# Kernel tuning notes

Measured on AMD Instinct MI355X. Metric: run time of the kernel, lower is better.

The kernel has to match this reference:

```python
import jax, jax.numpy as jnp
import numpy as np

HEADS = 16


def bemm(x, weight, bias, er, es):
    # BatchEnsembleMM.forward: x [T,B,Hin], weight [Hout,Hin], er [B,Hin], es [B,Hout]
    x_r = x * er[None, :, :]
    x_mm = jnp.einsum('tbh,oh->tbo', x_r, weight)
    return x_mm * es[None, :, :] + bias


def rel_shift(x):
    # RelativeShift.forward (batch_first): x [N, len_q, len_r]
    n, q, r = x.shape
    x_pad = jnp.pad(x, ((0, 0), (0, 0), (1, 0)))        # [N, q, r+1]
    x_view = x_pad.reshape(n, r + 1, q)[:, 1:, :]        # drop first 'row'
    return x_view.reshape(n, q, r)


def setup_inputs() -> dict:
    key = jax.random.key(0)
    ks = jax.random.split(key, 14)
    T, B, H = 1024, 8, 1024
    Lr = 1024
    s = 0.02
    return {
        'inputs': jax.random.normal(ks[0], (T, B, H), jnp.float32),
        'pos': jax.random.normal(ks[1], (Lr, 1, H), jnp.float32),
        'input_weights': jax.random.normal(ks[2], (3 * H, H), jnp.float32) * s,
        'input_biases': jax.random.normal(ks[3], (3 * H,), jnp.float32) * s,
        'pos_weights': jax.random.normal(ks[4], (H, H), jnp.float32) * s,
        'pos_biases': jax.random.normal(ks[5], (H,), jnp.float32) * s,
        'output_weights': jax.random.normal(ks[6], (H, H), jnp.float32) * s,
        'output_biases': jax.random.normal(ks[7], (H,), jnp.float32) * s,
        'r_i': 1.0 + jax.random.normal(ks[8], (B, H), jnp.float32) * 0.1,
        's_i': 1.0 + jax.random.normal(ks[9], (B, 3 * H), jnp.float32) * 0.1,
        'r_p': 1.0 + jax.random.normal(ks[10], (B, H), jnp.float32) * 0.1,
        's_p': 1.0 + jax.random.normal(ks[11], (B, H), jnp.float32) * 0.1,
        'r_w_bias': jax.random.normal(ks[12], (HEADS, H // HEADS), jnp.float32) * s,
        'r_r_bias': jax.random.normal(ks[13], (HEADS, H // HEADS), jnp.float32) * s,
        'heads': HEADS,
    }


def reference(inputs, pos, input_weights, input_biases, pos_weights, pos_biases,
              output_weights, output_biases, r_i, s_i, r_p, s_p,
              r_w_bias, r_r_bias, heads):
    T, B, H = inputs.shape
    hd = H // heads
    scale = hd ** (-0.5)
    Lr = pos.shape[0]

    pos_rep = jnp.broadcast_to(pos, (Lr, B, H))

    # BatchEnsemble QKV and positional projections (training path)
    qkv = bemm(inputs, input_weights, input_biases, r_i, s_i)       # [T,B,3H]
    qkv = qkv.reshape(T, B * heads, 3, hd)
    queries, keys, values = qkv[:, :, 0, :], qkv[:, :, 1, :], qkv[:, :, 2, :]

    r_head_k = bemm(pos_rep, pos_weights, pos_biases, r_p, s_p)     # [Lr,B,H]
    r_head_k = r_head_k.reshape(Lr, B * heads, hd)

    rw_head_q = (queries.reshape(T, B, heads, hd) + r_w_bias).reshape(T, B * heads, hd)
    rr_head_q = (queries.reshape(T, B, heads, hd) + r_r_bias).reshape(T, B * heads, hd)

    # content score AC and position score BD
    matmul_ac = jnp.einsum('qnd,knd->nqk', rw_head_q, keys) * scale    # [B*h,T,T]
    matmul_bd = jnp.einsum('qnd,rnd->nqr', rr_head_q, r_head_k) * scale
    matmul_bd = rel_shift(matmul_bd)[:, :, :T]

    attn_score = matmul_ac + matmul_bd
    softmax_results = jax.nn.softmax(attn_score.astype(jnp.float32), axis=-1).astype(inputs.dtype)

    context = jnp.einsum('nqk,knd->qnd', softmax_results, values).reshape(T, B, H)
    outputs = jnp.einsum('tbh,oh->tbo', context, output_weights) + output_biases
    return outputs
```

## Files before the change

### kernel.cpp

```cpp
#include <hip/hip_runtime.h>
#include <cstdint>
#include <cstddef>

using u16 = unsigned short;
typedef short short8 __attribute__((ext_vector_type(8)));
typedef unsigned short us8 __attribute__((ext_vector_type(8)));
typedef unsigned short us4 __attribute__((ext_vector_type(4)));
typedef float f32x4 __attribute__((ext_vector_type(4)));
typedef float f4 __attribute__((ext_vector_type(4)));

#define T_ 1024
#define B_ 8
#define H_ 1024
#define HEADS_ 16
#define HD_ 64
#define N3_ 3072

__device__ __forceinline__ float b2f(u16 u){
  union { float f; unsigned int i; } v; v.i = ((unsigned int)u) << 16; return v.f;
}
__device__ __forceinline__ u16 f2b(float f){
  union { float f; unsigned int i; } v; v.f = f;
  return (u16)((v.i + 0x8000u) >> 16);
}

template<bool HAS_S, bool SCALE_A, bool POS_A, bool A_BF16, bool OUT_F32>
__global__ __launch_bounds__(256) void k_gemm(const void* __restrict__ A_, const float* __restrict__ W,
                                              const float* __restrict__ RA, const float* __restrict__ S,
                                              const float* __restrict__ bias, void* __restrict__ C_, int N){
  const int K = 1024;
  const int n0 = blockIdx.x * 128, m0 = blockIdx.y * 128;
  const int tid = threadIdx.x, lane = tid & 63;
  const int wave = tid >> 6, wr = wave >> 1, wc = wave & 1;
  __shared__ alignas(16) u16 At[128 * 32];
  __shared__ alignas(16) u16 Bt[128 * 32];
  f32x4 acc[4][4] = {};

  for (int kt = 0; kt < 32; ++kt){
    const int k0 = kt * 32;
    f4 wv[4];
    us8 avb[2];
    f4 avf[4];
#pragma unroll
    for (int i = 0; i < 4; ++i){
      int c = tid + i * 256, r = c >> 3, sg = c & 7;
      wv[i] = *(const f4*)(W + (size_t)(n0 + r) * K + k0 + sg * 4);
    }
    if (A_BF16){
      const u16* A = (const u16*)A_;
#pragma unroll
      for (int i = 0; i < 2; ++i){
        int c = tid + i * 256, r = c >> 2, sg = c & 3;
        avb[i] = *(const us8*)(A + (size_t)(m0 + r) * K + k0 + sg * 8);
      }
    } else {
      const float* A = (const float*)A_;
#pragma unroll
      for (int i = 0; i < 4; ++i){
        int c = tid + i * 256, r = c >> 3, sg = c & 7;
        int m = m0 + r;
        const float* ap = POS_A ? (A + (size_t)(m >> 3) * K + k0 + sg * 4)
                                : (A + (size_t)m * K + k0 + sg * 4);
        avf[i] = *(const f4*)ap;
        if (SCALE_A){
          f4 rv = *(const f4*)(RA + (m & 7) * K + k0 + sg * 4);
          avf[i] = avf[i] * rv;
        }
      }
    }
    __syncthreads();
#pragma unroll
    for (int i = 0; i < 4; ++i){
      int c = tid + i * 256, r = c >> 3, sg = c & 7;
      us4 pw;
#pragma unroll
      for (int u = 0; u < 4; ++u) pw[u] = f2b(wv[i][u]);
      *(us4*)(Bt + r * 32 + sg * 4) = pw;
    }
    if (A_BF16){
#pragma unroll
      for (int i = 0; i < 2; ++i){
        int c = tid + i * 256, r = c >> 2, sg = c & 3;
        *(us8*)(At + r * 32 + sg * 8) = avb[i];
      }
    } else {
#pragma unroll
      for (int i = 0; i < 4; ++i){
        int c = tid + i * 256, r = c >> 3, sg = c & 7;
        us4 pa;
#pragma unroll
        for (int u = 0; u < 4; ++u) pa[u] = f2b(avf[i][u]);
        *(us4*)(At + r * 32 + sg * 4) = pa;
      }
    }
    __syncthreads();
    short8 af[4], bf[4];
#pragma unroll
    for (int i = 0; i < 4; ++i){
      int ar = wr * 64 + i * 16 + (lane & 15);
      af[i] = *(const short8*)(At + ar * 32 + ((lane >> 4) << 3));
      int br = wc * 64 + i * 16 + (lane & 15);
      bf[i] = *(const short8*)(Bt + br * 32 + ((lane >> 4) << 3));
    }
#pragma unroll
    for (int i = 0; i < 4; ++i)
#pragma unroll
      for (int j = 0; j < 4; ++j)
        acc[i][j] = __builtin_amdgcn_mfma_f32_16x16x32_bf16(af[i], bf[j], acc[i][j], 0, 0, 0);
  }
#pragma unroll
  for (int i = 0; i < 4; ++i){
    int row0 = wr * 64 + i * 16 + ((lane >> 4) << 2);
#pragma unroll
    for (int j = 0; j < 4; ++j){
      int o = n0 + wc * 64 + j * 16 + (lane & 15);
      float bv = bias[o];
#pragma unroll
      for (int jj = 0; jj < 4; ++jj){
        int m = m0 + row0 + jj;
        float v = acc[i][j][jj];
        if (HAS_S) v *= S[(m & 7) * N + o];
        v += bv;
        if (OUT_F32) ((float*)C_)[(size_t)m * N + o] = v;
        else         ((u16*)C_)[(size_t)m * N + o] = f2b(v);
      }
    }
  }
}

__global__ __launch_bounds__(256) void k_vt(const u16* __restrict__ qkv, u16* __restrict__ VT){
  const int tt = blockIdx.x;
  const int n = blockIdx.y;
  const int b = n >> 4, head = n & 15;
  __shared__ alignas(16) u16 tile[64][72];
  const int tid = threadIdx.x;
#pragma unroll
  for (int i = 0; i < 2; ++i){
    int c = tid + i * 256;
    int r = c >> 3, sg = c & 7;
    const u16* src = qkv + ((size_t)(tt * 64 + r) * 8 + b) * N3_ + head * 192 + 128 + sg * 8;
    *(us8*)&tile[r][sg * 8] = *(const us8*)src;
  }
  __syncthreads();
#pragma unroll
  for (int i = 0; i < 2; ++i){
    int c = tid + i * 256;
    int d = c >> 3, sg = c & 7;
    us8 ov;
#pragma unroll
    for (int u = 0; u < 8; ++u) ov[u] = tile[sg * 8 + u][d];
    *(us8*)(VT + ((size_t)n * 64 + d) * 1024 + tt * 64 + sg * 8) = ov;
  }
}

#define G_OFF   0
#define KV_OFF  67856
#define RWQ_OFF 133392
#define RRQ_OFF 137488
#define RED_OFF 143632
#define SMEM_SZ 145808

__device__ __forceinline__ int gswz(int byt){ return byt ^ (((byt >> 13) & 3) << 5); }

__global__ __launch_bounds__(512, 1) void k_attn(const u16* __restrict__ qkv, const u16* __restrict__ rk,
                                                 const u16* __restrict__ VTg, const float* __restrict__ rwb,
                                                 const float* __restrict__ rrb, u16* __restrict__ ctx){
  const int bid = blockIdx.x;
  const int n = (bid & 7) + ((bid >> 8) << 3);
  const int qb = (bid >> 3) & 31;
  const int q0 = qb * 32;
  const int bat = n >> 4, head = n & 15;
  const int tid = threadIdx.x, lane = tid & 63, wave = tid >> 6;
  const int l15 = lane & 15, grp = lane >> 4;

  __shared__ alignas(16) char smem[SMEM_SZ];
  char* gB  = smem + G_OFF;
  char* kvS = smem + KV_OFF;
  u16* rwq = (u16*)(smem + RWQ_OFF);
  u16* rrq = (u16*)(smem + RRQ_OFF);
  float* redf = (float*)(smem + RED_OFF);

  us8 stv[8];

#pragma unroll
  for (int i = 0; i < 8; ++i){ int c = tid + i * 512, r = c >> 3, sg = c & 7;
    stv[i] = *(const us8*)(rk + ((size_t)r * 8 + bat) * 1024 + head * 64 + sg * 8); }

  const float PRESCALE = 0.125f * 1.44269504089f;
#pragma unroll
  for (int rep = 0; rep < 2; ++rep){
    int c = tid + rep * 512;
    if (c < 640){
      int s = c >> 3, sg = c & 7;
      u16* dst; int row; const float* bias;
      if (s < 32){ dst = rwq; row = s; bias = rwb; }
      else       { dst = rrq; row = s - 32; bias = rrb; }
      int qrow = q0 + row;
      float v[8];
      const float* bp2 = bias + head * 64 + sg * 8;
      if (qrow < T_){
        const u16* qp = qkv + ((size_t)qrow * 8 + bat) * N3_ + head * 192 + sg * 8;
        us8 qv = *(const us8*)qp;
        f4 b0 = *(const f4*)bp2, b1 = *(const f4*)(bp2 + 4);
#pragma unroll
        for (int u = 0; u < 4; ++u){
          v[u]     = (b2f(qv[u])     + b0[u]) * PRESCALE;
          v[u + 4] = (b2f(qv[u + 4]) + b1[u]) * PRESCALE;
        }
      } else {
#pragma unroll
        for (int u = 0; u < 8; ++u) v[u] = 0.f;
      }
      us8 pk;
#pragma unroll
      for (int u = 0; u < 8; ++u) pk[u] = f2b(v[u]);
      *(us8*)((char*)dst + row * 128 + ((sg * 16) ^ ((row & 7) << 4))) = pk;
    }
  }
  if (tid < 33) *(u16*)(gB + gswz(tid * 2050 + 2048)) = 0;

  auto ldf = [&](const void* base, int row, int kkb)->short8 {
    int co = kkb + (grp << 4);
    return *(const short8*)((const char*)base + row * 128 + (co ^ ((row & 7) << 4)));
  };
  auto stageKV = [&](){
#pragma unroll
    for (int i = 0; i < 8; ++i){ int c = tid + i * 512, r = c >> 3, sg = c & 7;
      *(us8*)(kvS + r * 128 + ((sg * 16) ^ ((r & 7) << 4))) = stv[i]; }
  };
  auto computeB = [&](int s){
    short8 af[3][2];
#pragma unroll
    for (int pi = 0; pi < 3; ++pi)
#pragma unroll
      for (int kk = 0; kk < 2; ++kk) af[pi][kk] = ldf(rrq, pi * 16 + l15, kk * 64);
#pragma unroll
    for (int c4 = 0; c4 < 4; ++c4){
      int brow = wave * 64 + c4 * 16 + l15;
      short8 bf0 = ldf(kvS, brow, 0), bf1 = ldf(kvS, brow, 64);
      int rg = s * 512 + wave * 64 + c4 * 16 + l15;
#pragma unroll
      for (int pi = 0; pi < 3; ++pi){
        f32x4 acc = {0.f, 0.f, 0.f, 0.f};
        acc = __builtin_amdgcn_mfma_f32_16x16x32_bf16(af[pi][0], bf0, acc, 0, 0, 0);
        acc = __builtin_amdgcn_mfma_f32_16x16x32_bf16(af[pi][1], bf1, acc, 0, 0, 0);
#pragma unroll
        for (int jj = 0; jj < 4; ++jj){
          int a = pi * 16 + (grp << 2) + jj;
          if (a < 33) *(u16*)(gB + gswz(a * 2050 + (rg << 1))) = f2b(acc[jj]);
        }
      }
    }
  };

  __syncthreads();
  stageKV();
#pragma unroll
  for (int i = 0; i < 8; ++i){ int c = tid + i * 512, r = c >> 3, sg = c & 7;
    stv[i] = *(const us8*)(rk + ((size_t)(512 + r) * 8 + bat) * 1024 + head * 64 + sg * 8); }
  __syncthreads();
  computeB(0);
  __syncthreads();
  stageKV();
#pragma unroll
  for (int i = 0; i < 8; ++i){ int c = tid + i * 512, r = c >> 3, sg = c & 7;
    stv[i] = *(const us8*)(qkv + ((size_t)r * 8 + bat) * N3_ + head * 192 + 64 + sg * 8); }
  __syncthreads();
  computeB(1);

  f32x4 p[2][2][4];
  float pm[2][4];
#pragma unroll
  for (int m = 0; m < 2; ++m)
#pragma unroll
    for (int jj = 0; jj < 4; ++jj) pm[m][jj] = -3.0e38f;

  auto computeC = [&](int s){
    short8 af[2][2];
#pragma unroll
    for (int m = 0; m < 2; ++m)
#pragma unroll
      for (int kk = 0; kk < 2; ++kk) af[m][kk] = ldf(rwq, m * 16 + l15, kk * 64);
#pragma unroll
    for (int c4 = 0; c4 < 4; ++c4){
      int brow = wave * 64 + c4 * 16 + l15;
      short8 bf0 = ldf(kvS, brow, 0), bf1 = ldf(kvS, brow, 64);
      int bcol = s * 512 + wave * 64 + c4 * 16 + l15;
      int byt0 = ((1023 - q0 + bcol) << 1) + (grp << 13);
#pragma unroll
      for (int m = 0; m < 2; ++m){
        f32x4 acc = {0.f, 0.f, 0.f, 0.f};
        acc = __builtin_amdgcn_mfma_f32_16x16x32_bf16(af[m][0], bf0, acc, 0, 0, 0);
        acc = __builtin_amdgcn_mfma_f32_16x16x32_bf16(af[m][1], bf1, acc, 0, 0, 0);
#pragma unroll
        for (int jj = 0; jj < 4; ++jj){
          int byt = byt0 + (m << 15) + (jj << 11);
          float gv = b2f(*(const u16*)(gB + gswz(byt)));
          float sc = acc[jj] + gv;
          p[s][m][c4][jj] = sc;
          pm[m][jj] = fmaxf(pm[m][jj], sc);
        }
      }
    }
  };

  __syncthreads();
  stageKV();
#pragma unroll
  for (int i = 0; i < 8; ++i){ int c = tid + i * 512, r = c >> 3, sg = c & 7;
    stv[i] = *(const us8*)(qkv + ((size_t)(512 + r) * 8 + bat) * N3_ + head * 192 + 64 + sg * 8); }
  __syncthreads();
  computeC(0);
  __syncthreads();
  stageKV();
  __syncthreads();
  computeC(1);

#pragma unroll
  for (int m = 0; m < 2; ++m)
#pragma unroll
    for (int jj = 0; jj < 4; ++jj)
#pragma unroll
      for (int mk = 1; mk < 16; mk <<= 1) pm[m][jj] = fmaxf(pm[m][jj], __shfl_xor(pm[m][jj], mk));
  __syncthreads();
#pragma unroll
  for (int i = 0; i < 8; ++i){ int c = tid + i * 512, d = c >> 6, tc = c & 63;
    stv[i] = *(const us8*)(VTg + ((size_t)n * 64 + d) * 1024 + tc * 8); }
  if (l15 == 0){
#pragma unroll
    for (int m = 0; m < 2; ++m)
#pragma unroll
      for (int jj = 0; jj < 4; ++jj) redf[wave * 32 + m * 16 + (grp << 2) + jj] = pm[m][jj];
  }
  __syncthreads();
  float M_[2][4];
#pragma unroll
  for (int m = 0; m < 2; ++m)
#pragma unroll
    for (int jj = 0; jj < 4; ++jj){
      int row = m * 16 + (grp << 2) + jj;
      float v = redf[row];
#pragma unroll
      for (int w = 1; w < 8; ++w) v = fmaxf(v, redf[w * 32 + row]);
      M_[m][jj] = v;
    }
#pragma unroll
  for (int i = 0; i < 8; ++i){ int c = tid + i * 512, d = c >> 6, tc = c & 63;
    *(us8*)(kvS + d * 1024 + ((tc * 16) ^ ((d & 31) << 4))) = stv[i]; }
#pragma unroll
  for (int i = 0; i < 8; ++i){ int c = tid + i * 512, d = c >> 6, tc = c & 63;
    stv[i] = *(const us8*)(VTg + ((size_t)n * 64 + d) * 1024 + 512 + tc * 8); }

  float L_[2][4] = {};
#pragma unroll
  for (int s = 0; s < 2; ++s)
#pragma unroll
    for (int m = 0; m < 2; ++m)
#pragma unroll
      for (int c4 = 0; c4 < 4; ++c4)
#pragma unroll
        for (int jj = 0; jj < 4; ++jj){
          float e = __builtin_exp2f(p[s][m][c4][jj] - M_[m][jj]);
          p[s][m][c4][jj] = e;
          L_[m][jj] += e;
        }
#pragma unroll
  for (int m = 0; m < 2; ++m)
#pragma unroll
    for (int jj = 0; jj < 4; ++jj)
#pragma unroll
      for (int mk = 1; mk < 16; mk <<= 1) L_[m][jj] += __shfl_xor(L_[m][jj], mk);
  if (l15 == 0){
#pragma unroll
    for (int m = 0; m < 2; ++m)
#pragma unroll
      for (int jj = 0; jj < 4; ++jj) redf[256 + wave * 32 + m * 16 + (grp << 2) + jj] = L_[m][jj];
  }
  __syncthreads();
  if (wave == 0 && l15 == 0){
#pragma unroll
    for (int m = 0; m < 2; ++m)
#pragma unroll
      for (int jj = 0; jj < 4; ++jj){
        int row = m * 16 + (grp << 2) + jj;
        float sum = 0.f;
#pragma unroll
        for (int w = 0; w < 8; ++w) sum += redf[256 + w * 32 + row];
        redf[512 + row] = 1.0f / (sum + 1e-20f);
      }
  }

  char* ptW = smem + G_OFF + wave * 8192;
#pragma unroll
  for (int s = 0; s < 2; ++s)
#pragma unroll
    for (int m = 0; m < 2; ++m)
#pragma unroll
      for (int c4 = 0; c4 < 4; ++c4)
#pragma unroll
        for (int jj = 0; jj < 4; ++jj){
          int q = m * 16 + (grp << 2) + jj;
          int tl = s * 64 + c4 * 16 + l15;
          *(u16*)(ptW + q * 256 + ((tl * 2) ^ ((q & 7) << 4))) = f2b(p[s][m][c4][jj]);
        }
  __syncthreads();

  f32x4 Oacc[2][4] = {};
#pragma unroll
  for (int s = 0; s < 2; ++s){
#pragma unroll
    for (int kk = 0; kk < 2; ++kk){
      short8 pa[2];
#pragma unroll
      for (int m = 0; m < 2; ++m)
        pa[m] = *(const short8*)(ptW + (m * 16 + l15) * 256 + ((s * 128 + kk * 64 + (grp << 4)) ^ ((l15 & 7) << 4)));
#pragma unroll
      for (int dt = 0; dt < 4; ++dt){
        int dr = dt * 16 + l15;
        short8 vb = *(const short8*)(kvS + dr * 1024 + ((wave * 128 + kk * 64 + (grp << 4)) ^ ((dr & 31) << 4)));
#pragma unroll
        for (int m = 0; m < 2; ++m)
          Oacc[m][dt] = __builtin_amdgcn_mfma_f32_16x16x32_bf16(pa[m], vb, Oacc[m][dt], 0, 0, 0);
      }
    }
    if (s == 0){
      __syncthreads();
#pragma unroll
      for (int i = 0; i < 8; ++i){ int c = tid + i * 512, d = c >> 6, tc = c & 63;
        *(us8*)(kvS + d * 1024 + ((tc * 16) ^ ((d & 31) << 4))) = stv[i]; }
      __syncthreads();
    }
  }

  __syncthreads();
  float* par = (float*)kvS;
#pragma unroll
  for (int m = 0; m < 2; ++m)
#pragma unroll
    for (int dt = 0; dt < 4; ++dt)
#pragma unroll
      for (int jj = 0; jj < 4; ++jj)
        par[wave * 2048 + (m * 16 + (grp << 2) + jj) * 64 + dt * 16 + l15] = Oacc[m][dt][jj];
  __syncthreads();
  {
    f32x4 v = {0.f, 0.f, 0.f, 0.f};
#pragma unroll
    for (int w = 0; w < 8; ++w) v += *(const f32x4*)(par + w * 2048 + tid * 4);
    int q = tid >> 4, d4 = (tid & 15) * 4;
    float il = redf[512 + q];
    us4 pk;
#pragma unroll
    for (int e = 0; e < 4; ++e) pk[e] = f2b(v[e] * il);
    *(us4*)(ctx + ((size_t)(q0 + q) * 8 + bat) * 1024 + head * 64 + d4) = pk;
  }
}

extern "C" void kernel_launch(void* const* d_in, const int* in_sizes, int n_in,
                              void* d_out, int out_size, void* d_ws, size_t ws_size,
                              hipStream_t stream){
  const float* x   = (const float*)d_in[0];
  const float* pos = (const float*)d_in[1];
  const float* Wi  = (const float*)d_in[2];
  const float* bi  = (const float*)d_in[3];
  const float* Wp  = (const float*)d_in[4];
  const float* bp  = (const float*)d_in[5];
  const float* Wo  = (const float*)d_in[6];
  const float* bo  = (const float*)d_in[7];
  const float* r_i = (const float*)d_in[8];
  const float* s_i = (const float*)d_in[9];
  const float* r_p = (const float*)d_in[10];
  const float* s_p = (const float*)d_in[11];
  const float* rwb = (const float*)d_in[12];
  const float* rrb = (const float*)d_in[13];

  const size_t MB = 1024 * 1024;
  u16* qkv = (u16*)((char*)d_ws);
  u16* rk  = (u16*)((char*)d_ws + 48 * MB);
  u16* VTg  = (u16*)d_out;
  u16* ctxg = (u16*)((char*)d_out + 16777216);

  k_gemm<true,  true,  false, false, false><<<dim3(24, 64), 256, 0, stream>>>(x,   Wi, r_i, s_i, bi, qkv, N3_);
  k_gemm<true,  true,  true,  false, false><<<dim3(8, 64),  256, 0, stream>>>(pos, Wp, r_p, s_p, bp, rk, 1024);
  k_vt<<<dim3(16, 128), 256, 0, stream>>>(qkv, VTg);
  k_attn<<<dim3(4096), 512, 0, stream>>>(qkv, rk, VTg, rwb, rrb, ctxg);
  hipMemcpyAsync(qkv, ctxg, (size_t)out_size * sizeof(u16), hipMemcpyDeviceToDevice, stream);
  k_gemm<false, false, false, true, true><<<dim3(8, 64), 256, 0, stream>>>(qkv, Wo, nullptr, nullptr, bo, (float*)d_out, 1024);
}
```

Before: 455.2 us.

## Load K, R and V fragments directly from global memory, dropping LDS staging

```diff
diff --git a/kernel.cpp b/kernel.cpp
--- a/kernel.cpp
+++ b/kernel.cpp
@@ -154,15 +154,14 @@
 }
 
 #define G_OFF   0
-#define KV_OFF  67856
-#define RWQ_OFF 133392
-#define RRQ_OFF 137488
-#define RED_OFF 143632
-#define SMEM_SZ 145808
+#define RWQ_OFF 67664
+#define RRQ_OFF 71760
+#define RED_OFF 77904
+#define SMEM_SZ 79952
 
 __device__ __forceinline__ int gswz(int byt){ return byt ^ (((byt >> 13) & 3) << 5); }
 
-__global__ __launch_bounds__(512, 1) void k_attn(const u16* __restrict__ qkv, const u16* __restrict__ rk,
+__global__ __launch_bounds__(512, 4) void k_attn(const u16* __restrict__ qkv, const u16* __restrict__ rk,
                                                  const u16* __restrict__ VTg, const float* __restrict__ rwb,
                                                  const float* __restrict__ rrb, u16* __restrict__ ctx){
   const int bid = blockIdx.x;
@@ -175,16 +174,9 @@
 
   __shared__ alignas(16) char smem[SMEM_SZ];
   char* gB  = smem + G_OFF;
-  char* kvS = smem + KV_OFF;
   u16* rwq = (u16*)(smem + RWQ_OFF);
   u16* rrq = (u16*)(smem + RRQ_OFF);
   float* redf = (float*)(smem + RED_OFF);
-
-  us8 stv[8];
-
-#pragma unroll
-  for (int i = 0; i < 8; ++i){ int c = tid + i * 512, r = c >> 3, sg = c & 7;
-    stv[i] = *(const us8*)(rk + ((size_t)r * 8 + bat) * 1024 + head * 64 + sg * 8); }
 
   const float PRESCALE = 0.125f * 1.44269504089f;
 #pragma unroll
@@ -223,12 +215,11 @@
     int co = kkb + (grp << 4);
     return *(const short8*)((const char*)base + row * 128 + (co ^ ((row & 7) << 4)));
   };
-  auto stageKV = [&](){
-#pragma unroll
-    for (int i = 0; i < 8; ++i){ int c = tid + i * 512, r = c >> 3, sg = c & 7;
-      *(us8*)(kvS + r * 128 + ((sg * 16) ^ ((r & 7) << 4))) = stv[i]; }
-  };
-  auto computeB = [&](int s){
+
+  __syncthreads();
+
+#pragma unroll
+  for (int s = 0; s < 2; ++s){
     short8 af[3][2];
 #pragma unroll
     for (int pi = 0; pi < 3; ++pi)
@@ -236,8 +227,10 @@
       for (int kk = 0; kk < 2; ++kk) af[pi][kk] = ldf(rrq, pi * 16 + l15, kk * 64);
 #pragma unroll
     for (int c4 = 0; c4 < 4; ++c4){
-      int brow = wave * 64 + c4 * 16 + l15;
-      short8 bf0 = ldf(kvS, brow, 0), bf1 = ldf(kvS, brow, 64);
+      int r = s * 512 + wave * 64 + c4 * 16 + l15;
+      const u16* bp = rk + ((size_t)r * 8 + bat) * 1024 + head * 64 + grp * 8;
+      short8 bf0 = *(const short8*)bp;
+      short8 bf1 = *(const short8*)(bp + 32);
       int rg = s * 512 + wave * 64 + c4 * 16 + l15;
 #pragma unroll
       for (int pi = 0; pi < 3; ++pi){
@@ -251,22 +244,8 @@
         }
       }
     }
-  };
-
-  __syncthreads();
-  stageKV();
-#pragma unroll
-  for (int i = 0; i < 8; ++i){ int c = tid + i * 512, r = c >> 3, sg = c & 7;
-    stv[i] = *(const us8*)(rk + ((size_t)(512 + r) * 8 + bat) * 1024 + head * 64 + sg * 8); }
-  __syncthreads();
-  computeB(0);
-  __syncthreads();
-  stageKV();
-#pragma unroll
-  for (int i = 0; i < 8; ++i){ int c = tid + i * 512, r = c >> 3, sg = c & 7;
-    stv[i] = *(const us8*)(qkv + ((size_t)r * 8 + bat) * N3_ + head * 192 + 64 + sg * 8); }
-  __syncthreads();
-  computeB(1);
+  }
+  __syncthreads();
 
   f32x4 p[2][2][4];
   float pm[2][4];
@@ -275,7 +254,8 @@
 #pragma unroll
     for (int jj = 0; jj < 4; ++jj) pm[m][jj] = -3.0e38f;
 
-  auto computeC = [&](int s){
+#pragma unroll
+  for (int s = 0; s < 2; ++s){
     short8 af[2][2];
 #pragma unroll
     for (int m = 0; m < 2; ++m)
@@ -283,9 +263,10 @@
       for (int kk = 0; kk < 2; ++kk) af[m][kk] = ldf(rwq, m * 16 + l15, kk * 64);
 #pragma unroll
     for (int c4 = 0; c4 < 4; ++c4){
-      int brow = wave * 64 + c4 * 16 + l15;
-      short8 bf0 = ldf(kvS, brow, 0), bf1 = ldf(kvS, brow, 64);
       int bcol = s * 512 + wave * 64 + c4 * 16 + l15;
+      const u16* kp = qkv + ((size_t)bcol * 8 + bat) * N3_ + head * 192 + 64 + grp * 8;
+      short8 bf0 = *(const short8*)kp;
+      short8 bf1 = *(const short8*)(kp + 32);
       int byt0 = ((1023 - q0 + bcol) << 1) + (grp << 13);
 #pragma unroll
       for (int m = 0; m < 2; ++m){
@@ -302,19 +283,7 @@
         }
       }
     }
-  };
-
-  __syncthreads();
-  stageKV();
-#pragma unroll
-  for (int i = 0; i < 8; ++i){ int c = tid + i * 512, r = c >> 3, sg = c & 7;
-    stv[i] = *(const us8*)(qkv + ((size_t)(512 + r) * 8 + bat) * N3_ + head * 192 + 64 + sg * 8); }
-  __syncthreads();
-  computeC(0);
-  __syncthreads();
-  stageKV();
-  __syncthreads();
-  computeC(1);
+  }
 
 #pragma unroll
   for (int m = 0; m < 2; ++m)
@@ -322,10 +291,6 @@
     for (int jj = 0; jj < 4; ++jj)
 #pragma unroll
       for (int mk = 1; mk < 16; mk <<= 1) pm[m][jj] = fmaxf(pm[m][jj], __shfl_xor(pm[m][jj], mk));
-  __syncthreads();
-#pragma unroll
-  for (int i = 0; i < 8; ++i){ int c = tid + i * 512, d = c >> 6, tc = c & 63;
-    stv[i] = *(const us8*)(VTg + ((size_t)n * 64 + d) * 1024 + tc * 8); }
   if (l15 == 0){
 #pragma unroll
     for (int m = 0; m < 2; ++m)
@@ -344,13 +309,8 @@
       for (int w = 1; w < 8; ++w) v = fmaxf(v, redf[w * 32 + row]);
       M_[m][jj] = v;
     }
-#pragma unroll
-  for (int i = 0; i < 8; ++i){ int c = tid + i * 512, d = c >> 6, tc = c & 63;
-    *(us8*)(kvS + d * 1024 + ((tc * 16) ^ ((d & 31) << 4))) = stv[i]; }
-#pragma unroll
-  for (int i = 0; i < 8; ++i){ int c = tid + i * 512, d = c >> 6, tc = c & 63;
-    stv[i] = *(const us8*)(VTg + ((size_t)n * 64 + d) * 1024 + 512 + tc * 8); }
-
+
+  char* ptW = smem + G_OFF + wave * 8192;
   float L_[2][4] = {};
 #pragma unroll
   for (int s = 0; s < 2; ++s)
@@ -361,8 +321,10 @@
 #pragma unroll
         for (int jj = 0; jj < 4; ++jj){
           float e = __builtin_exp2f(p[s][m][c4][jj] - M_[m][jj]);
-          p[s][m][c4][jj] = e;
           L_[m][jj] += e;
+          int q = m * 16 + (grp << 2) + jj;
+          int tl = s * 64 + c4 * 16 + l15;
+          *(u16*)(ptW + q * 256 + ((tl * 2) ^ ((q & 7) << 4))) = f2b(e);
         }
 #pragma unroll
   for (int m = 0; m < 2; ++m)
@@ -377,33 +339,6 @@
       for (int jj = 0; jj < 4; ++jj) redf[256 + wave * 32 + m * 16 + (grp << 2) + jj] = L_[m][jj];
   }
   __syncthreads();
-  if (wave == 0 && l15 == 0){
-#pragma unroll
-    for (int m = 0; m < 2; ++m)
-#pragma unroll
-      for (int jj = 0; jj < 4; ++jj){
-        int row = m * 16 + (grp << 2) + jj;
-        float sum = 0.f;
-#pragma unroll
-        for (int w = 0; w < 8; ++w) sum += redf[256 + w * 32 + row];
-        redf[512 + row] = 1.0f / (sum + 1e-20f);
-      }
-  }
-
-  char* ptW = smem + G_OFF + wave * 8192;
-#pragma unroll
-  for (int s = 0; s < 2; ++s)
-#pragma unroll
-    for (int m = 0; m < 2; ++m)
-#pragma unroll
-      for (int c4 = 0; c4 < 4; ++c4)
-#pragma unroll
-        for (int jj = 0; jj < 4; ++jj){
-          int q = m * 16 + (grp << 2) + jj;
-          int tl = s * 64 + c4 * 16 + l15;
-          *(u16*)(ptW + q * 256 + ((tl * 2) ^ ((q & 7) << 4))) = f2b(p[s][m][c4][jj]);
-        }
-  __syncthreads();
 
   f32x4 Oacc[2][4] = {};
 #pragma unroll
@@ -414,40 +349,37 @@
 #pragma unroll
       for (int m = 0; m < 2; ++m)
         pa[m] = *(const short8*)(ptW + (m * 16 + l15) * 256 + ((s * 128 + kk * 64 + (grp << 4)) ^ ((l15 & 7) << 4)));
+      int tg = s * 512 + wave * 64 + kk * 32 + grp * 8;
 #pragma unroll
       for (int dt = 0; dt < 4; ++dt){
         int dr = dt * 16 + l15;
-        short8 vb = *(const short8*)(kvS + dr * 1024 + ((wave * 128 + kk * 64 + (grp << 4)) ^ ((dr & 31) << 4)));
+        short8 vb = *(const short8*)(VTg + ((size_t)n * 64 + dr) * 1024 + tg);
 #pragma unroll
         for (int m = 0; m < 2; ++m)
           Oacc[m][dt] = __builtin_amdgcn_mfma_f32_16x16x32_bf16(pa[m], vb, Oacc[m][dt], 0, 0, 0);
       }
     }
-    if (s == 0){
-      __syncthreads();
-#pragma unroll
-      for (int i = 0; i < 8; ++i){ int c = tid + i * 512, d = c >> 6, tc = c & 63;
-        *(us8*)(kvS + d * 1024 + ((tc * 16) ^ ((d & 31) << 4))) = stv[i]; }
-      __syncthreads();
-    }
-  }
-
-  __syncthreads();
-  float* par = (float*)kvS;
+  }
+
+  float* par = (float*)ptW;
 #pragma unroll
   for (int m = 0; m < 2; ++m)
 #pragma unroll
     for (int dt = 0; dt < 4; ++dt)
 #pragma unroll
       for (int jj = 0; jj < 4; ++jj)
-        par[wave * 2048 + (m * 16 + (grp << 2) + jj) * 64 + dt * 16 + l15] = Oacc[m][dt][jj];
+        par[(m * 16 + (grp << 2) + jj) * 64 + dt * 16 + l15] = Oacc[m][dt][jj];
   __syncthreads();
   {
+    float* parAll = (float*)(smem + G_OFF);
     f32x4 v = {0.f, 0.f, 0.f, 0.f};
 #pragma unroll
-    for (int w = 0; w < 8; ++w) v += *(const f32x4*)(par + w * 2048 + tid * 4);
+    for (int w = 0; w < 8; ++w) v += *(const f32x4*)(parAll + w * 2048 + tid * 4);
     int q = tid >> 4, d4 = (tid & 15) * 4;
-    float il = redf[512 + q];
+    float sum = 0.f;
+#pragma unroll
+    for (int w = 0; w < 8; ++w) sum += redf[256 + w * 32 + q];
+    float il = 1.0f / (sum + 1e-20f);
     us4 pk;
 #pragma unroll
     for (int e = 0; e < 4; ++e) pk[e] = f2b(v[e] * il);
```

After: 427.9 us. -6.0%, faster.
